# Performance work log

Measured on AMD Instinct MI355X. Metric: run time of the kernel, lower is better.

The kernel has to match this reference:

```python
import jax, jax.numpy as jnp
import numpy as np

C = 256
CI = C // 2  # inter_channels


def conv1x1(x, w, b):
    # x: [B,C,H,W], w: [O,C], b: [O] -> [B,O,H,W]
    return jnp.einsum('bchw,oc->bohw', x, w) + b[None, :, None, None]


def setup_inputs() -> dict:
    key = jax.random.key(0)
    ks = jax.random.split(key, 9)
    B, H, W = 8, 56, 56
    s = 0.02
    return {
        'x': jax.random.normal(ks[0], (B, C, H, W), dtype=jnp.float32),
        'g_w': jax.random.normal(ks[1], (CI, C), dtype=jnp.float32) * s,
        'g_b': jax.random.normal(ks[2], (CI,), dtype=jnp.float32) * s,
        'theta_w': jax.random.normal(ks[3], (CI, C), dtype=jnp.float32) * s,
        'theta_b': jax.random.normal(ks[4], (CI,), dtype=jnp.float32) * s,
        'phi_w': jax.random.normal(ks[5], (CI, C), dtype=jnp.float32) * s,
        'phi_b': jax.random.normal(ks[6], (CI,), dtype=jnp.float32) * s,
        'W_w': jax.random.normal(ks[7], (C, CI), dtype=jnp.float32) * s,
        'W_b': jax.random.normal(ks[8], (C,), dtype=jnp.float32) * s,
    }


def reference(x, g_w, g_b, theta_w, theta_b, phi_w, phi_b, W_w, W_b):
    B, Cc, H, Wd = x.shape
    N = H * Wd
    g_x = conv1x1(x, g_w, g_b).reshape(B, CI, N).transpose(0, 2, 1)        # [B,N,CI]
    theta_x = conv1x1(x, theta_w, theta_b).reshape(B, CI, N).transpose(0, 2, 1)  # [B,N,CI]
    phi_x = conv1x1(x, phi_w, phi_b).reshape(B, CI, N)                     # [B,CI,N]
    f = jnp.einsum('bnc,bcm->bnm', theta_x, phi_x)                         # [B,N,N]
    attn = jax.nn.softmax(f, axis=-1)
    y = jnp.einsum('bnm,bmc->bnc', attn, g_x)                              # [B,N,CI]
    y = y.transpose(0, 2, 1).reshape(B, CI, H, Wd)                         # [B,CI,H,W]
    z = conv1x1(y, W_w, W_b) + x
    return z
```

## Files before the change

kernel.cpp:

```cpp
#include <hip/hip_runtime.h>

#define NB 8
#define C 256
#define CI 128
#define NPIX 3136
#define NT 64
#define NTILES 49
#define NGQ 13
#define NROWT 98
#define NSPLIT 4
#define LOG2E 1.44269504f

typedef unsigned short u16;
typedef unsigned int u32;
typedef __bf16 bf16x8 __attribute__((ext_vector_type(8)));
typedef float f32x4 __attribute__((ext_vector_type(4)));
typedef float f32x16 __attribute__((ext_vector_type(16)));

static __device__ __forceinline__ u16 f2b(float f) {
  union { float f; u32 u; } v; v.f = f;
  u32 r = v.u + 0x7FFFu + ((v.u >> 16) & 1u);
  return (u16)(r >> 16);
}
static __device__ __forceinline__ float b2f(u16 v) {
  union { u32 u; float f; } x; x.u = ((u32)v) << 16; return x.f;
}
static __device__ __forceinline__ u32 cvtpk(float lo, float hi) {
  u32 r;
  asm("v_cvt_pk_bf16_f32 %0, %1, %2" : "=v"(r) : "v"(lo), "v"(hi));
  return r;
}
static __device__ __forceinline__ void swap32(u32& x, u32& y) {
  asm("v_permlane32_swap_b32 %0, %1" : "+v"(x), "+v"(y));
}
static __device__ __forceinline__ void gl16(const void* g, void* l) {
  __builtin_amdgcn_global_load_lds(
      (const __attribute__((address_space(1))) u32*)g,
      (__attribute__((address_space(3))) u32*)l, 16, 0, 0);
}

__global__ __launch_bounds__(256) void k0_convert(
    const float* __restrict__ g_w, const float* __restrict__ th_w,
    const float* __restrict__ ph_w, const float* __restrict__ W_w,
    u16* __restrict__ wcat, u16* __restrict__ Wbf) {
  int i = blockIdx.x * 256 + threadIdx.x;
  if (i < 98304) {
    int o = i >> 8, c = i & 255;
    float v = (o < 128) ? g_w[o * 256 + c]
            : (o < 256) ? th_w[(o - 128) * 256 + c] * LOG2E
                        : ph_w[(o - 256) * 256 + c];
    wcat[i] = f2b(v);
  } else {
    int j = i - 98304;
    Wbf[j] = f2b(W_w[j]);
  }
}

__global__ __launch_bounds__(256) void k1_proj(
    const float* __restrict__ x, const float* __restrict__ g_b,
    const float* __restrict__ th_b, const float* __restrict__ ph_b,
    const u16* __restrict__ wcat, u16* __restrict__ thO,
    u16* __restrict__ phO, u16* __restrict__ gO) {
  __shared__ __align__(16) u16 xT[32 * 264];
  char* xTb = reinterpret_cast<char*>(xT);
  int tid = threadIdx.x;
  int b = blockIdx.x / NROWT, nt = blockIdx.x % NROWT;
  int n0 = nt * 32;
  const float* xb = x + (size_t)b * C * NPIX;
  {
    int c0 = tid >> 3, nq = tid & 7;
    for (int k = 0; k < 8; ++k) {
      int c = c0 + 32 * k;
      float4 xv = *reinterpret_cast<const float4*>(xb + (size_t)c * NPIX + n0 + 4 * nq);
      float vals[4] = {xv.x, xv.y, xv.z, xv.w};
#pragma unroll
      for (int j = 0; j < 4; ++j) {
        int row = 4 * nq + j;
        xT[row * 264 + c] = f2b(vals[j]);
      }
    }
  }
  __syncthreads();
  int wave = tid >> 6, lane = tid & 63;
  int wq = wave & 1, wo = wave >> 1;
  int r = 16 * wq + (lane & 15);
  bf16x8 a[8];
#pragma unroll
  for (int kk = 0; kk < 8; ++kk) {
    int ch = 4 * kk + (lane >> 4);
    a[kk] = *reinterpret_cast<const bf16x8*>(xTb + r * 528 + ch * 16);
  }
  for (int os = 12 * wo; os < 12 * wo + 12; ++os) {
    int o = 16 * os + (lane & 15);
    f32x4 acc = {0.f, 0.f, 0.f, 0.f};
    const u16* wrow = wcat + (size_t)o * 256 + 8 * (lane >> 4);
#pragma unroll
    for (int kk = 0; kk < 8; ++kk) {
      bf16x8 bb = *reinterpret_cast<const bf16x8*>(wrow + 32 * kk);
      acc = __builtin_amdgcn_mfma_f32_16x16x32_bf16(a[kk], bb, acc, 0, 0, 0);
    }
    int p = os >> 3;
    int ol = (os & 7) * 16 + (lane & 15);
    const float* bias = (p == 0) ? g_b : (p == 1) ? th_b : ph_b;
    float bv = bias[ol];
    if (p == 1) bv *= LOG2E;
    int nbase = n0 + 16 * wq + 4 * (lane >> 4);
    if (p == 0) {
      ushort4 pk;
      pk.x = f2b(acc[0] + bv); pk.y = f2b(acc[1] + bv);
      pk.z = f2b(acc[2] + bv); pk.w = f2b(acc[3] + bv);
      *reinterpret_cast<ushort4*>(gO + ((size_t)b * CI + ol) * NPIX + nbase) = pk;
    } else {
      u16* dst = (p == 1) ? thO : phO;
#pragma unroll
      for (int j = 0; j < 4; ++j)
        dst[((size_t)b * NPIX + nbase + j) * CI + ol] = f2b(acc[j] + bv);
    }
  }
}

__global__ __launch_bounds__(512, 2) void k2_attn(
    const u16* __restrict__ th, const u16* __restrict__ ph,
    const u16* __restrict__ gbuf, u16* __restrict__ yp,
    float* __restrict__ lm) {
  __shared__ __align__(16) char lds[65536];
  int tid = threadIdx.x, wave = tid >> 6, lane = tid & 63;
  int h5 = lane >> 5, l31 = lane & 31;
  int bid = blockIdx.x;
  int s = bid & 3, rest = bid >> 2;
  int b = rest / NGQ, ng = rest % NGQ;
  int qbase = ng * 256 + wave * 32;
  if (qbase + 32 > NPIX) qbase = NPIX - 32;
  int ts = (NTILES * s) >> 2, te = (NTILES * (s + 1)) >> 2;

  bf16x8 bth[8];
  {
    const u16* trow = th + ((size_t)b * NPIX + qbase + l31) * CI;
#pragma unroll
    for (int ks = 0; ks < 8; ++ks)
      bth[ks] = *reinterpret_cast<const bf16x8*>(trow + 16 * ks + 8 * h5);
  }
  float lrun = 0.f;
  f32x16 zv;
#pragma unroll
  for (int j = 0; j < 16; ++j) zv[j] = 0.f;
  f32x16 yacc[4];
#pragma unroll
  for (int cb = 0; cb < 4; ++cb)
#pragma unroll
    for (int j = 0; j < 16; ++j) yacc[cb][j] = 0.f;

  auto stage = [&](int buf, int mt) {
    int m0 = mt * NT;
    char* phB = lds + buf * 16384;
    char* gB = lds + 32768 + buf * 16384;
#pragma unroll
    for (int c = 0; c < 2; ++c) {
      int call = wave * 2 + c;
      int o = call * 1024 + lane * 16;
      int row = o >> 8, chl = (o >> 4) & 15;
      int chg = chl ^ (row & 15);
      gl16(ph + ((size_t)(b * NPIX + m0 + row)) * CI + chg * 8, phB + call * 1024);
    }
#pragma unroll
    for (int c = 0; c < 2; ++c) {
      int call = wave * 2 + c;
      int o = call * 1024 + lane * 16;
      int ci = o >> 7, chl = (o >> 4) & 7;
      int chg = chl ^ (ci & 7);
      gl16(gbuf + ((size_t)b * CI + ci) * NPIX + m0 + chg * 8, gB + call * 1024);
    }
  };

  stage(0, ts);
  int cur = 0;
  for (int mt = ts; mt < te; ++mt) {
    bool pre = (mt + 1 < te);
    if (pre) stage(cur ^ 1, mt + 1);
    if (pre) {
      asm volatile("s_waitcnt vmcnt(4)" ::: "memory");
    } else {
      asm volatile("s_waitcnt vmcnt(0)" ::: "memory");
    }
    __builtin_amdgcn_s_barrier();
    __builtin_amdgcn_sched_barrier(0);
    char* phB = lds + cur * 16384;
    char* gB = lds + 32768 + cur * 16384;
    f32x16 sv0, sv1;
    __builtin_amdgcn_s_setprio(1);
    {
      int off = l31 * 256 + ((h5 ^ (l31 & 15)) << 4);
      bf16x8 a0 = *reinterpret_cast<const bf16x8*>(phB + off);
      bf16x8 a1 = *reinterpret_cast<const bf16x8*>(phB + off + 8192);
      sv0 = __builtin_amdgcn_mfma_f32_32x32x16_bf16(a0, bth[0], zv, 0, 0, 0);
      sv1 = __builtin_amdgcn_mfma_f32_32x32x16_bf16(a1, bth[0], zv, 0, 0, 0);
    }
#pragma unroll
    for (int ks = 1; ks < 8; ++ks) {
      int chk = 2 * ks + h5;
      int off = l31 * 256 + ((chk ^ (l31 & 15)) << 4);
      bf16x8 a0 = *reinterpret_cast<const bf16x8*>(phB + off);
      bf16x8 a1 = *reinterpret_cast<const bf16x8*>(phB + off + 8192);
      sv0 = __builtin_amdgcn_mfma_f32_32x32x16_bf16(a0, bth[ks], sv0, 0, 0, 0);
      sv1 = __builtin_amdgcn_mfma_f32_32x32x16_bf16(a1, bth[ks], sv1, 0, 0, 0);
    }
    __builtin_amdgcn_s_setprio(0);
#pragma unroll
    for (int j = 0; j < 16; ++j) {
      sv0[j] = exp2f(sv0[j]);
      sv1[j] = exp2f(sv1[j]);
    }
    float a0 = 0.f, a1 = 0.f, a2 = 0.f, a3 = 0.f;
#pragma unroll
    for (int i = 0; i < 16; i += 4) {
      a0 += sv0[i] + sv1[i];
      a1 += sv0[i + 1] + sv1[i + 1];
      a2 += sv0[i + 2] + sv1[i + 2];
      a3 += sv0[i + 3] + sv1[i + 3];
    }
    lrun += (a0 + a1) + (a2 + a3);
    u32 pk[2][4][2];
#pragma unroll
    for (int t = 0; t < 4; ++t) {
      pk[0][t][0] = cvtpk(sv0[4 * t], sv0[4 * t + 1]);
      pk[0][t][1] = cvtpk(sv0[4 * t + 2], sv0[4 * t + 3]);
      pk[1][t][0] = cvtpk(sv1[4 * t], sv1[4 * t + 1]);
      pk[1][t][1] = cvtpk(sv1[4 * t + 2], sv1[4 * t + 3]);
    }
    __builtin_amdgcn_s_setprio(1);
#pragma unroll
    for (int ks = 0; ks < 4; ++ks) {
      int m2 = ks >> 1, t0 = 2 * (ks & 1);
      swap32(pk[m2][t0][0], pk[m2][t0 + 1][0]);
      swap32(pk[m2][t0][1], pk[m2][t0 + 1][1]);
      union { u32 u[4]; bf16x8 v; } f;
      f.u[0] = pk[m2][t0][0]; f.u[1] = pk[m2][t0][1];
      f.u[2] = pk[m2][t0 + 1][0]; f.u[3] = pk[m2][t0 + 1][1];
      int chk = 2 * ks + h5;
#pragma unroll
      for (int cb = 0; cb < 4; ++cb) {
        int ci = 32 * cb + l31;
        bf16x8 gv = *reinterpret_cast<const bf16x8*>(
            gB + ci * 128 + ((chk ^ (ci & 7)) << 4));
        yacc[cb] = __builtin_amdgcn_mfma_f32_32x32x16_bf16(f.v, gv, yacc[cb], 0, 0, 0);
      }
    }
    __builtin_amdgcn_s_setprio(0);
    __builtin_amdgcn_sched_barrier(0);
    asm volatile("s_waitcnt lgkmcnt(0)" ::: "memory");
    __builtin_amdgcn_s_barrier();
    cur ^= 1;
  }
  lrun += __shfl_xor(lrun, 32);
  u16* ypb = yp + (size_t)(s * NB + b) * NPIX * CI;
#pragma unroll
  for (int cb = 0; cb < 4; ++cb)
#pragma unroll
    for (int j = 0; j < 16; ++j) {
      int n = qbase + (j & 3) + 8 * (j >> 2) + 4 * h5;
      ypb[(size_t)n * CI + 32 * cb + l31] = f2b(yacc[cb][j]);
    }
  if (lane < 32) {
    int n = qbase + l31;
    lm[(size_t)(s * NB + b) * NPIX + n] = lrun;
  }
}

__global__ __launch_bounds__(256) void k3_out(
    const u16* __restrict__ yp, const float* __restrict__ lm,
    const u16* __restrict__ Wbf, const float* __restrict__ W_b,
    const float* __restrict__ x, float* __restrict__ z) {
  int tid = threadIdx.x, wave = tid >> 6, lane = tid & 63;
  int b = blockIdx.x / NROWT, nt = blockIdx.x % NROWT;
  int n0 = nt * 32;
  int q = lane >> 4, l15 = lane & 15;
  int wq = wave & 1, wo = wave >> 1;
  int nfr = n0 + 16 * wq + l15;
  float den = 0.f;
#pragma unroll
  for (int s = 0; s < NSPLIT; ++s)
    den += lm[(size_t)(s * NB + b) * NPIX + nfr];
  float inv = 1.f / den;
  bf16x8 a[4];
#pragma unroll
  for (int kk = 0; kk < 4; ++kk) {
    float ac[8];
#pragma unroll
    for (int e = 0; e < 8; ++e) ac[e] = 0.f;
#pragma unroll
    for (int s = 0; s < NSPLIT; ++s) {
      union { uint4 u4; u16 us[8]; } yv;
      yv.u4 = *reinterpret_cast<const uint4*>(
          yp + (size_t)(s * NB + b) * NPIX * CI + (size_t)nfr * CI + 32 * kk + 8 * q);
#pragma unroll
      for (int e = 0; e < 8; ++e) ac[e] += b2f(yv.us[e]);
    }
    union { u32 u[4]; bf16x8 v; } fa;
    fa.u[0] = cvtpk(ac[0] * inv, ac[1] * inv);
    fa.u[1] = cvtpk(ac[2] * inv, ac[3] * inv);
    fa.u[2] = cvtpk(ac[4] * inv, ac[5] * inv);
    fa.u[3] = cvtpk(ac[6] * inv, ac[7] * inv);
    a[kk] = fa.v;
  }
  for (int os = 8 * wo; os < 8 * wo + 8; ++os) {
    int co = 16 * os + l15;
    f32x4 acc = {0.f, 0.f, 0.f, 0.f};
    const u16* wrow = Wbf + (size_t)co * 128 + 8 * q;
#pragma unroll
    for (int kk = 0; kk < 4; ++kk) {
      bf16x8 bb = *reinterpret_cast<const bf16x8*>(wrow + 32 * kk);
      acc = __builtin_amdgcn_mfma_f32_16x16x32_bf16(a[kk], bb, acc, 0, 0, 0);
    }
    float bw = W_b[co];
    int nb = n0 + 16 * wq + 4 * q;
    size_t off = ((size_t)b * C + co) * NPIX + nb;
    float4 xv = *reinterpret_cast<const float4*>(x + off);
    float4 o;
    o.x = acc[0] + bw + xv.x; o.y = acc[1] + bw + xv.y;
    o.z = acc[2] + bw + xv.z; o.w = acc[3] + bw + xv.w;
    *reinterpret_cast<float4*>(z + off) = o;
  }
}

extern "C" void kernel_launch(void* const* d_in, const int* in_sizes, int n_in,
                              void* d_out, int out_size, void* d_ws, size_t ws_size,
                              hipStream_t stream) {
  const float* x    = (const float*)d_in[0];
  const float* g_w  = (const float*)d_in[1];
  const float* g_b  = (const float*)d_in[2];
  const float* th_w = (const float*)d_in[3];
  const float* th_b = (const float*)d_in[4];
  const float* ph_w = (const float*)d_in[5];
  const float* ph_b = (const float*)d_in[6];
  const float* W_w  = (const float*)d_in[7];
  const float* W_b  = (const float*)d_in[8];
  float* z = (float*)d_out;
  u16* ws = (u16*)d_ws;
  u16* wcat = ws;
  u16* Wbf  = ws + 98304;
  u16* th   = ws + 131072;
  u16* phb  = th + 3211264;
  u16* gbb  = phb + 3211264;
  u16* yp   = gbb + 3211264;
  float* lm = (float*)(ws + 131072 + (size_t)3211264 * 7);
  hipLaunchKernelGGL(k0_convert, dim3(512), dim3(256), 0, stream,
                     g_w, th_w, ph_w, W_w, wcat, Wbf);
  hipLaunchKernelGGL(k1_proj, dim3(NB * NROWT), dim3(256), 0, stream,
                     x, g_b, th_b, ph_b, wcat, th, phb, gbb);
  hipLaunchKernelGGL(k2_attn, dim3(NB * NGQ * NSPLIT), dim3(512), 0, stream,
                     th, phb, gbb, yp, lm);
  hipLaunchKernelGGL(k3_out, dim3(NB * NROWT), dim3(256), 0, stream,
                     yp, lm, Wbf, W_b, x, z);
}
```

Before: 150.8 us.

## Software-pipeline QK^T of next tile with softmax/PV of current tile in attention

The attention kernel now computes the QK^T scores for tile t+1 while doing exp, packing and the PV MFMAs for tile t. It stages phi two tiles ahead and g one tile ahead, using separate staging lambdas. Blocks shrink from 512 to 256 threads (128 queries per block, 25 groups per batch) and the two-blocks-per-CU launch bound is dropped. The aim is to hide MFMA and global-load latency behind the exp work, at the cost of more registers for the second score buffer and more blocks each loading the same K/V tiles.

```diff
diff --git a/kernel.cpp b/kernel.cpp
--- a/kernel.cpp
+++ b/kernel.cpp
@@ -6,7 +6,7 @@
 #define NPIX 3136
 #define NT 64
 #define NTILES 49
-#define NGQ 13
+#define NG 25
 #define NROWT 98
 #define NSPLIT 4
 #define LOG2E 1.44269504f
@@ -119,7 +119,7 @@
   }
 }
 
-__global__ __launch_bounds__(512, 2) void k2_attn(
+__global__ __launch_bounds__(256) void k2_attn(
     const u16* __restrict__ th, const u16* __restrict__ ph,
     const u16* __restrict__ gbuf, u16* __restrict__ yp,
     float* __restrict__ lm) {
@@ -128,8 +128,8 @@
   int h5 = lane >> 5, l31 = lane & 31;
   int bid = blockIdx.x;
   int s = bid & 3, rest = bid >> 2;
-  int b = rest / NGQ, ng = rest % NGQ;
-  int qbase = ng * 256 + wave * 32;
+  int b = rest / NG, ng = rest % NG;
+  int qbase = ng * 128 + wave * 32;
   if (qbase + 32 > NPIX) qbase = NPIX - 32;
   int ts = (NTILES * s) >> 2, te = (NTILES * (s + 1)) >> 2;
 
@@ -150,50 +150,39 @@
 #pragma unroll
     for (int j = 0; j < 16; ++j) yacc[cb][j] = 0.f;
 
-  auto stage = [&](int buf, int mt) {
+  auto stage_phi = [&](int buf, int mt) {
     int m0 = mt * NT;
     char* phB = lds + buf * 16384;
-    char* gB = lds + 32768 + buf * 16384;
-#pragma unroll
-    for (int c = 0; c < 2; ++c) {
-      int call = wave * 2 + c;
+#pragma unroll
+    for (int c = 0; c < 4; ++c) {
+      int call = wave * 4 + c;
       int o = call * 1024 + lane * 16;
       int row = o >> 8, chl = (o >> 4) & 15;
       int chg = chl ^ (row & 15);
       gl16(ph + ((size_t)(b * NPIX + m0 + row)) * CI + chg * 8, phB + call * 1024);
     }
-#pragma unroll
-    for (int c = 0; c < 2; ++c) {
-      int call = wave * 2 + c;
+  };
+  auto stage_g = [&](int buf, int mt) {
+    int m0 = mt * NT;
+    char* gB = lds + 32768 + buf * 16384;
+#pragma unroll
+    for (int c = 0; c < 4; ++c) {
+      int call = wave * 4 + c;
       int o = call * 1024 + lane * 16;
       int ci = o >> 7, chl = (o >> 4) & 7;
       int chg = chl ^ (ci & 7);
       gl16(gbuf + ((size_t)b * CI + ci) * NPIX + m0 + chg * 8, gB + call * 1024);
     }
   };
-
-  stage(0, ts);
-  int cur = 0;
-  for (int mt = ts; mt < te; ++mt) {
-    bool pre = (mt + 1 < te);
-    if (pre) stage(cur ^ 1, mt + 1);
-    if (pre) {
-      asm volatile("s_waitcnt vmcnt(4)" ::: "memory");
-    } else {
-      asm volatile("s_waitcnt vmcnt(0)" ::: "memory");
-    }
-    __builtin_amdgcn_s_barrier();
-    __builtin_amdgcn_sched_barrier(0);
-    char* phB = lds + cur * 16384;
-    char* gB = lds + 32768 + cur * 16384;
-    f32x16 sv0, sv1;
+  auto qk = [&](int buf, f32x16& s0, f32x16& s1) {
+    char* phB = lds + buf * 16384;
     __builtin_amdgcn_s_setprio(1);
     {
       int off = l31 * 256 + ((h5 ^ (l31 & 15)) << 4);
       bf16x8 a0 = *reinterpret_cast<const bf16x8*>(phB + off);
       bf16x8 a1 = *reinterpret_cast<const bf16x8*>(phB + off + 8192);
-      sv0 = __builtin_amdgcn_mfma_f32_32x32x16_bf16(a0, bth[0], zv, 0, 0, 0);
-      sv1 = __builtin_amdgcn_mfma_f32_32x32x16_bf16(a1, bth[0], zv, 0, 0, 0);
+      s0 = __builtin_amdgcn_mfma_f32_32x32x16_bf16(a0, bth[0], zv, 0, 0, 0);
+      s1 = __builtin_amdgcn_mfma_f32_32x32x16_bf16(a1, bth[0], zv, 0, 0, 0);
     }
 #pragma unroll
     for (int ks = 1; ks < 8; ++ks) {
@@ -201,32 +190,42 @@
       int off = l31 * 256 + ((chk ^ (l31 & 15)) << 4);
       bf16x8 a0 = *reinterpret_cast<const bf16x8*>(phB + off);
       bf16x8 a1 = *reinterpret_cast<const bf16x8*>(phB + off + 8192);
-      sv0 = __builtin_amdgcn_mfma_f32_32x32x16_bf16(a0, bth[ks], sv0, 0, 0, 0);
-      sv1 = __builtin_amdgcn_mfma_f32_32x32x16_bf16(a1, bth[ks], sv1, 0, 0, 0);
+      s0 = __builtin_amdgcn_mfma_f32_32x32x16_bf16(a0, bth[ks], s0, 0, 0, 0);
+      s1 = __builtin_amdgcn_mfma_f32_32x32x16_bf16(a1, bth[ks], s1, 0, 0, 0);
     }
     __builtin_amdgcn_s_setprio(0);
+  };
+  auto body = [&](int t, f32x16& c0, f32x16& c1, f32x16& n0v, f32x16& n1v) {
+    asm volatile("s_waitcnt vmcnt(0)" ::: "memory");
+    __builtin_amdgcn_s_barrier();
+    __builtin_amdgcn_sched_barrier(0);
+    int p = (t - ts) & 1;
+    if (t + 1 < te) stage_g(p ^ 1, t + 1);
+    if (t + 2 < te) stage_phi(p, t + 2);
+    if (t + 1 < te) qk(p ^ 1, n0v, n1v);
 #pragma unroll
     for (int j = 0; j < 16; ++j) {
-      sv0[j] = exp2f(sv0[j]);
-      sv1[j] = exp2f(sv1[j]);
+      c0[j] = exp2f(c0[j]);
+      c1[j] = exp2f(c1[j]);
     }
     float a0 = 0.f, a1 = 0.f, a2 = 0.f, a3 = 0.f;
 #pragma unroll
     for (int i = 0; i < 16; i += 4) {
-      a0 += sv0[i] + sv1[i];
-      a1 += sv0[i + 1] + sv1[i + 1];
-      a2 += sv0[i + 2] + sv1[i + 2];
-      a3 += sv0[i + 3] + sv1[i + 3];
+      a0 += c0[i] + c1[i];
+      a1 += c0[i + 1] + c1[i + 1];
+      a2 += c0[i + 2] + c1[i + 2];
+      a3 += c0[i + 3] + c1[i + 3];
     }
     lrun += (a0 + a1) + (a2 + a3);
     u32 pk[2][4][2];
 #pragma unroll
-    for (int t = 0; t < 4; ++t) {
-      pk[0][t][0] = cvtpk(sv0[4 * t], sv0[4 * t + 1]);
-      pk[0][t][1] = cvtpk(sv0[4 * t + 2], sv0[4 * t + 3]);
-      pk[1][t][0] = cvtpk(sv1[4 * t], sv1[4 * t + 1]);
-      pk[1][t][1] = cvtpk(sv1[4 * t + 2], sv1[4 * t + 3]);
-    }
+    for (int tt = 0; tt < 4; ++tt) {
+      pk[0][tt][0] = cvtpk(c0[4 * tt], c0[4 * tt + 1]);
+      pk[0][tt][1] = cvtpk(c0[4 * tt + 2], c0[4 * tt + 3]);
+      pk[1][tt][0] = cvtpk(c1[4 * tt], c1[4 * tt + 1]);
+      pk[1][tt][1] = cvtpk(c1[4 * tt + 2], c1[4 * tt + 3]);
+    }
+    char* gB = lds + 32768 + p * 16384;
     __builtin_amdgcn_s_setprio(1);
 #pragma unroll
     for (int ks = 0; ks < 4; ++ks) {
@@ -246,11 +245,26 @@
       }
     }
     __builtin_amdgcn_s_setprio(0);
-    __builtin_amdgcn_sched_barrier(0);
-    asm volatile("s_waitcnt lgkmcnt(0)" ::: "memory");
-    __builtin_amdgcn_s_barrier();
-    cur ^= 1;
-  }
+  };
+
+  f32x16 sA0, sA1, sB0, sB1;
+  stage_phi(0, ts);
+  stage_g(0, ts);
+  if (ts + 1 < te) {
+    stage_phi(1, ts + 1);
+    asm volatile("s_waitcnt vmcnt(8)" ::: "memory");
+  } else {
+    asm volatile("s_waitcnt vmcnt(4)" ::: "memory");
+  }
+  __builtin_amdgcn_s_barrier();
+  __builtin_amdgcn_sched_barrier(0);
+  qk(0, sA0, sA1);
+
+  for (int t = ts; t < te; t += 2) {
+    body(t, sA0, sA1, sB0, sB1);
+    if (t + 1 < te) body(t + 1, sB0, sB1, sA0, sA1);
+  }
+
   lrun += __shfl_xor(lrun, 32);
   u16* ypb = yp + (size_t)(s * NB + b) * NPIX * CI;
 #pragma unroll
@@ -347,7 +361,7 @@
                      g_w, th_w, ph_w, W_w, wcat, Wbf);
   hipLaunchKernelGGL(k1_proj, dim3(NB * NROWT), dim3(256), 0, stream,
                      x, g_b, th_b, ph_b, wcat, th, phb, gbb);
-  hipLaunchKernelGGL(k2_attn, dim3(NB * NGQ * NSPLIT), dim3(512), 0, stream,
+  hipLaunchKernelGGL(k2_attn, dim3(NB * NG * NSPLIT), dim3(256), 0, stream,
                      th, phb, gbb, yp, lm);
   hipLaunchKernelGGL(k3_out, dim3(NB * NROWT), dim3(256), 0, stream,
                      yp, lm, Wbf, W_b, x, z);
```

Measured after the change: 180.9 us. 20.0% more time.

## Read phi directly from global and shrink attention blocks to four waves

Applied to the files above, without the earlier changes.

The attention kernel no longer stages phi tiles in LDS. Each wave loads its phi fragments straight from global memory, and only the g tile is double-buffered in LDS. The block is halved to 256 threads covering 128 queries with a 32KB LDS footprint, which doubles the grid. The g prefetch is moved after the QK^T MFMAs and the trailing per-iteration barrier is dropped, cutting LDS traffic and synchronisation. In exchange, phi is now read redundantly by every wave through L1/L2 with uncoalesced row-strided loads, and the last query group overlaps with its neighbour and recomputes some rows.

```diff
diff --git a/kernel.cpp b/kernel.cpp
--- a/kernel.cpp
+++ b/kernel.cpp
@@ -6,7 +6,7 @@
 #define NPIX 3136
 #define NT 64
 #define NTILES 49
-#define NGQ 13
+#define NG 25
 #define NROWT 98
 #define NSPLIT 4
 #define LOG2E 1.44269504f
@@ -119,17 +119,17 @@
   }
 }
 
-__global__ __launch_bounds__(512, 2) void k2_attn(
+__global__ __launch_bounds__(256) void k2_attn(
     const u16* __restrict__ th, const u16* __restrict__ ph,
     const u16* __restrict__ gbuf, u16* __restrict__ yp,
     float* __restrict__ lm) {
-  __shared__ __align__(16) char lds[65536];
+  __shared__ __align__(16) char lds[32768];
   int tid = threadIdx.x, wave = tid >> 6, lane = tid & 63;
   int h5 = lane >> 5, l31 = lane & 31;
   int bid = blockIdx.x;
   int s = bid & 3, rest = bid >> 2;
-  int b = rest / NGQ, ng = rest % NGQ;
-  int qbase = ng * 256 + wave * 32;
+  int b = rest / NG, ng = rest % NG;
+  int qbase = ng * 128 + wave * 32;
   if (qbase + 32 > NPIX) qbase = NPIX - 32;
   int ts = (NTILES * s) >> 2, te = (NTILES * (s + 1)) >> 2;
 
@@ -150,21 +150,12 @@
 #pragma unroll
     for (int j = 0; j < 16; ++j) yacc[cb][j] = 0.f;
 
-  auto stage = [&](int buf, int mt) {
+  auto stage_g = [&](int buf, int mt) {
     int m0 = mt * NT;
-    char* phB = lds + buf * 16384;
-    char* gB = lds + 32768 + buf * 16384;
-#pragma unroll
-    for (int c = 0; c < 2; ++c) {
-      int call = wave * 2 + c;
-      int o = call * 1024 + lane * 16;
-      int row = o >> 8, chl = (o >> 4) & 15;
-      int chg = chl ^ (row & 15);
-      gl16(ph + ((size_t)(b * NPIX + m0 + row)) * CI + chg * 8, phB + call * 1024);
-    }
-#pragma unroll
-    for (int c = 0; c < 2; ++c) {
-      int call = wave * 2 + c;
+    char* gB = lds + buf * 16384;
+#pragma unroll
+    for (int c = 0; c < 4; ++c) {
+      int call = wave * 4 + c;
       int o = call * 1024 + lane * 16;
       int ci = o >> 7, chl = (o >> 4) & 7;
       int chg = chl ^ (ci & 7);
@@ -172,39 +163,35 @@
     }
   };
 
-  stage(0, ts);
+  stage_g(0, ts);
   int cur = 0;
   for (int mt = ts; mt < te; ++mt) {
-    bool pre = (mt + 1 < te);
-    if (pre) stage(cur ^ 1, mt + 1);
-    if (pre) {
-      asm volatile("s_waitcnt vmcnt(4)" ::: "memory");
-    } else {
-      asm volatile("s_waitcnt vmcnt(0)" ::: "memory");
-    }
+    asm volatile("s_waitcnt vmcnt(0)" ::: "memory");
     __builtin_amdgcn_s_barrier();
     __builtin_amdgcn_sched_barrier(0);
-    char* phB = lds + cur * 16384;
-    char* gB = lds + 32768 + cur * 16384;
+    const u16* phbase = ph + ((size_t)b * NPIX + mt * NT) * CI;
     f32x16 sv0, sv1;
     __builtin_amdgcn_s_setprio(1);
     {
-      int off = l31 * 256 + ((h5 ^ (l31 & 15)) << 4);
-      bf16x8 a0 = *reinterpret_cast<const bf16x8*>(phB + off);
-      bf16x8 a1 = *reinterpret_cast<const bf16x8*>(phB + off + 8192);
+      int chk = h5;
+      const u16* pr = phbase + l31 * CI + chk * 8;
+      bf16x8 a0 = *reinterpret_cast<const bf16x8*>(pr);
+      bf16x8 a1 = *reinterpret_cast<const bf16x8*>(pr + 32 * CI);
       sv0 = __builtin_amdgcn_mfma_f32_32x32x16_bf16(a0, bth[0], zv, 0, 0, 0);
       sv1 = __builtin_amdgcn_mfma_f32_32x32x16_bf16(a1, bth[0], zv, 0, 0, 0);
     }
 #pragma unroll
     for (int ks = 1; ks < 8; ++ks) {
       int chk = 2 * ks + h5;
-      int off = l31 * 256 + ((chk ^ (l31 & 15)) << 4);
-      bf16x8 a0 = *reinterpret_cast<const bf16x8*>(phB + off);
-      bf16x8 a1 = *reinterpret_cast<const bf16x8*>(phB + off + 8192);
+      const u16* pr = phbase + l31 * CI + chk * 8;
+      bf16x8 a0 = *reinterpret_cast<const bf16x8*>(pr);
+      bf16x8 a1 = *reinterpret_cast<const bf16x8*>(pr + 32 * CI);
       sv0 = __builtin_amdgcn_mfma_f32_32x32x16_bf16(a0, bth[ks], sv0, 0, 0, 0);
       sv1 = __builtin_amdgcn_mfma_f32_32x32x16_bf16(a1, bth[ks], sv1, 0, 0, 0);
     }
     __builtin_amdgcn_s_setprio(0);
+    __builtin_amdgcn_sched_barrier(0);
+    if (mt + 1 < te) stage_g(cur ^ 1, mt + 1);
 #pragma unroll
     for (int j = 0; j < 16; ++j) {
       sv0[j] = exp2f(sv0[j]);
@@ -227,6 +214,7 @@
       pk[1][t][0] = cvtpk(sv1[4 * t], sv1[4 * t + 1]);
       pk[1][t][1] = cvtpk(sv1[4 * t + 2], sv1[4 * t + 3]);
     }
+    char* gB = lds + cur * 16384;
     __builtin_amdgcn_s_setprio(1);
 #pragma unroll
     for (int ks = 0; ks < 4; ++ks) {
@@ -246,9 +234,6 @@
       }
     }
     __builtin_amdgcn_s_setprio(0);
-    __builtin_amdgcn_sched_barrier(0);
-    asm volatile("s_waitcnt lgkmcnt(0)" ::: "memory");
-    __builtin_amdgcn_s_barrier();
     cur ^= 1;
   }
   lrun += __shfl_xor(lrun, 32);
@@ -347,7 +332,7 @@
                      g_w, th_w, ph_w, W_w, wcat, Wbf);
   hipLaunchKernelGGL(k1_proj, dim3(NB * NROWT), dim3(256), 0, stream,
                      x, g_b, th_b, ph_b, wcat, th, phb, gbb);
-  hipLaunchKernelGGL(k2_attn, dim3(NB * NGQ * NSPLIT), dim3(512), 0, stream,
+  hipLaunchKernelGGL(k2_attn, dim3(NB * NG * NSPLIT), dim3(256), 0, stream,
                      th, phb, gbb, yp, lm);
   hipLaunchKernelGGL(k3_out, dim3(NB * NROWT), dim3(256), 0, stream,
                      yp, lm, Wbf, W_b, x, z);
```

After: 194.3 us. 28.9% more time.

## Shrink attention blocks, single-buffer g tile, and rewrite projection as per-wave kernel

Applied to the files above, without the earlier changes.

The projection kernel becomes one wave per 16-pixel column tile. It loads x directly into registers with strided scalar loads, drops the LDS transpose and swaps MFMA operand roles so output writes change layout. The attention kernel goes from 512 to 256 threads with 128 queries per block, so there are more blocks. Its g tile is now single-buffered and staged after the loop-top barrier, with split waitcnts so the phi GEMM overlaps the g load and the end-of-iteration barrier is removed. This reduces LDS use and aims for better occupancy and overlap, but it risks uncoalesced x loads, and the single-buffered g tile may be overwritten while slower waves are still reading the previous one.

```diff
diff --git a/kernel.cpp b/kernel.cpp
--- a/kernel.cpp
+++ b/kernel.cpp
@@ -6,7 +6,8 @@
 #define NPIX 3136
 #define NT 64
 #define NTILES 49
-#define NGQ 13
+#define NG 25
+#define NCOLT 196
 #define NROWT 98
 #define NSPLIT 4
 #define LOG2E 1.44269504f
@@ -56,80 +57,72 @@
   }
 }
 
-__global__ __launch_bounds__(256) void k1_proj(
+__global__ __launch_bounds__(64) void k1_proj(
     const float* __restrict__ x, const float* __restrict__ g_b,
     const float* __restrict__ th_b, const float* __restrict__ ph_b,
     const u16* __restrict__ wcat, u16* __restrict__ thO,
     u16* __restrict__ phO, u16* __restrict__ gO) {
-  __shared__ __align__(16) u16 xT[32 * 264];
-  char* xTb = reinterpret_cast<char*>(xT);
-  int tid = threadIdx.x;
-  int b = blockIdx.x / NROWT, nt = blockIdx.x % NROWT;
-  int n0 = nt * 32;
+  int lane = threadIdx.x;
+  int bid = blockIdx.x;
+  int b = bid / NCOLT, ct = bid % NCOLT;
+  int n0 = ct * 16;
+  int q = lane >> 4, l15 = lane & 15;
+  int n = n0 + l15;
   const float* xb = x + (size_t)b * C * NPIX;
-  {
-    int c0 = tid >> 3, nq = tid & 7;
-    for (int k = 0; k < 8; ++k) {
-      int c = c0 + 32 * k;
-      float4 xv = *reinterpret_cast<const float4*>(xb + (size_t)c * NPIX + n0 + 4 * nq);
-      float vals[4] = {xv.x, xv.y, xv.z, xv.w};
-#pragma unroll
-      for (int j = 0; j < 4; ++j) {
-        int row = 4 * nq + j;
-        xT[row * 264 + c] = f2b(vals[j]);
-      }
-    }
-  }
-  __syncthreads();
-  int wave = tid >> 6, lane = tid & 63;
-  int wq = wave & 1, wo = wave >> 1;
-  int r = 16 * wq + (lane & 15);
-  bf16x8 a[8];
+  bf16x8 xf[8];
 #pragma unroll
   for (int kk = 0; kk < 8; ++kk) {
-    int ch = 4 * kk + (lane >> 4);
-    a[kk] = *reinterpret_cast<const bf16x8*>(xTb + r * 528 + ch * 16);
-  }
-  for (int os = 12 * wo; os < 12 * wo + 12; ++os) {
-    int o = 16 * os + (lane & 15);
+    const float* xc = xb + (size_t)(32 * kk + 8 * q) * NPIX + n;
+    float v[8];
+#pragma unroll
+    for (int e = 0; e < 8; ++e) v[e] = xc[(size_t)e * NPIX];
+    union { u32 u[4]; bf16x8 v8; } p;
+    p.u[0] = cvtpk(v[0], v[1]); p.u[1] = cvtpk(v[2], v[3]);
+    p.u[2] = cvtpk(v[4], v[5]); p.u[3] = cvtpk(v[6], v[7]);
+    xf[kk] = p.v8;
+  }
+  for (int os = 0; os < 24; ++os) {
+    int p_ = os >> 3;
+    int olb = (os & 7) * 16;
     f32x4 acc = {0.f, 0.f, 0.f, 0.f};
-    const u16* wrow = wcat + (size_t)o * 256 + 8 * (lane >> 4);
+    const u16* wrow = wcat + (size_t)(16 * os + l15) * 256 + 8 * q;
 #pragma unroll
     for (int kk = 0; kk < 8; ++kk) {
-      bf16x8 bb = *reinterpret_cast<const bf16x8*>(wrow + 32 * kk);
-      acc = __builtin_amdgcn_mfma_f32_16x16x32_bf16(a[kk], bb, acc, 0, 0, 0);
-    }
-    int p = os >> 3;
-    int ol = (os & 7) * 16 + (lane & 15);
-    const float* bias = (p == 0) ? g_b : (p == 1) ? th_b : ph_b;
-    float bv = bias[ol];
-    if (p == 1) bv *= LOG2E;
-    int nbase = n0 + 16 * wq + 4 * (lane >> 4);
-    if (p == 0) {
+      bf16x8 aw = *reinterpret_cast<const bf16x8*>(wrow + 32 * kk);
+      acc = __builtin_amdgcn_mfma_f32_16x16x32_bf16(aw, xf[kk], acc, 0, 0, 0);
+    }
+    const float* bias = (p_ == 0) ? g_b : (p_ == 1) ? th_b : ph_b;
+    float4 bv = *reinterpret_cast<const float4*>(bias + olb + 4 * q);
+    if (p_ == 1) { bv.x *= LOG2E; bv.y *= LOG2E; bv.z *= LOG2E; bv.w *= LOG2E; }
+    if (p_ == 0) {
+      int o = olb + 4 * q;
+      u16* gb = gO + ((size_t)b * CI + o) * NPIX + n;
+      gb[0] = f2b(acc[0] + bv.x);
+      gb[NPIX] = f2b(acc[1] + bv.y);
+      gb[2 * NPIX] = f2b(acc[2] + bv.z);
+      gb[3 * NPIX] = f2b(acc[3] + bv.w);
+    } else {
+      u16* dst = (p_ == 1) ? thO : phO;
       ushort4 pk;
-      pk.x = f2b(acc[0] + bv); pk.y = f2b(acc[1] + bv);
-      pk.z = f2b(acc[2] + bv); pk.w = f2b(acc[3] + bv);
-      *reinterpret_cast<ushort4*>(gO + ((size_t)b * CI + ol) * NPIX + nbase) = pk;
-    } else {
-      u16* dst = (p == 1) ? thO : phO;
-#pragma unroll
-      for (int j = 0; j < 4; ++j)
-        dst[((size_t)b * NPIX + nbase + j) * CI + ol] = f2b(acc[j] + bv);
-    }
-  }
-}
-
-__global__ __launch_bounds__(512, 2) void k2_attn(
+      pk.x = f2b(acc[0] + bv.x); pk.y = f2b(acc[1] + bv.y);
+      pk.z = f2b(acc[2] + bv.z); pk.w = f2b(acc[3] + bv.w);
+      *reinterpret_cast<ushort4*>(dst + ((size_t)b * NPIX + n) * CI + olb + 4 * q) = pk;
+    }
+  }
+}
+
+__global__ __launch_bounds__(256) void k2_attn(
     const u16* __restrict__ th, const u16* __restrict__ ph,
     const u16* __restrict__ gbuf, u16* __restrict__ yp,
     float* __restrict__ lm) {
-  __shared__ __align__(16) char lds[65536];
+  __shared__ __align__(16) char lds[49152];
+  char* gB = lds + 32768;
   int tid = threadIdx.x, wave = tid >> 6, lane = tid & 63;
   int h5 = lane >> 5, l31 = lane & 31;
   int bid = blockIdx.x;
   int s = bid & 3, rest = bid >> 2;
-  int b = rest / NGQ, ng = rest % NGQ;
-  int qbase = ng * 256 + wave * 32;
+  int b = rest / NG, ng = rest % NG;
+  int qbase = ng * 128 + wave * 32;
   if (qbase + 32 > NPIX) qbase = NPIX - 32;
   int ts = (NTILES * s) >> 2, te = (NTILES * (s + 1)) >> 2;
 
@@ -150,21 +143,23 @@
 #pragma unroll
     for (int j = 0; j < 16; ++j) yacc[cb][j] = 0.f;
 
-  auto stage = [&](int buf, int mt) {
+  auto stage_phi = [&](int buf, int mt) {
     int m0 = mt * NT;
     char* phB = lds + buf * 16384;
-    char* gB = lds + 32768 + buf * 16384;
-#pragma unroll
-    for (int c = 0; c < 2; ++c) {
-      int call = wave * 2 + c;
+#pragma unroll
+    for (int c = 0; c < 4; ++c) {
+      int call = wave * 4 + c;
       int o = call * 1024 + lane * 16;
       int row = o >> 8, chl = (o >> 4) & 15;
       int chg = chl ^ (row & 15);
       gl16(ph + ((size_t)(b * NPIX + m0 + row)) * CI + chg * 8, phB + call * 1024);
     }
-#pragma unroll
-    for (int c = 0; c < 2; ++c) {
-      int call = wave * 2 + c;
+  };
+  auto stage_g = [&](int mt) {
+    int m0 = mt * NT;
+#pragma unroll
+    for (int c = 0; c < 4; ++c) {
+      int call = wave * 4 + c;
       int o = call * 1024 + lane * 16;
       int ci = o >> 7, chl = (o >> 4) & 7;
       int chg = chl ^ (ci & 7);
@@ -172,20 +167,21 @@
     }
   };
 
-  stage(0, ts);
+  stage_phi(0, ts);
   int cur = 0;
   for (int mt = ts; mt < te; ++mt) {
-    bool pre = (mt + 1 < te);
-    if (pre) stage(cur ^ 1, mt + 1);
-    if (pre) {
-      asm volatile("s_waitcnt vmcnt(4)" ::: "memory");
-    } else {
-      asm volatile("s_waitcnt vmcnt(0)" ::: "memory");
-    }
     __builtin_amdgcn_s_barrier();
     __builtin_amdgcn_sched_barrier(0);
+    stage_g(mt);
+    bool pre = (mt + 1 < te);
+    if (pre) stage_phi(cur ^ 1, mt + 1);
+    if (pre) {
+      asm volatile("s_waitcnt vmcnt(8)" ::: "memory");
+    } else {
+      asm volatile("s_waitcnt vmcnt(4)" ::: "memory");
+    }
+    __builtin_amdgcn_sched_barrier(0);
     char* phB = lds + cur * 16384;
-    char* gB = lds + 32768 + cur * 16384;
     f32x16 sv0, sv1;
     __builtin_amdgcn_s_setprio(1);
     {
@@ -227,6 +223,12 @@
       pk[1][t][0] = cvtpk(sv1[4 * t], sv1[4 * t + 1]);
       pk[1][t][1] = cvtpk(sv1[4 * t + 2], sv1[4 * t + 3]);
     }
+    if (pre) {
+      asm volatile("s_waitcnt vmcnt(4)" ::: "memory");
+    } else {
+      asm volatile("s_waitcnt vmcnt(0)" ::: "memory");
+    }
+    __builtin_amdgcn_sched_barrier(0);
     __builtin_amdgcn_s_setprio(1);
 #pragma unroll
     for (int ks = 0; ks < 4; ++ks) {
@@ -246,9 +248,6 @@
       }
     }
     __builtin_amdgcn_s_setprio(0);
-    __builtin_amdgcn_sched_barrier(0);
-    asm volatile("s_waitcnt lgkmcnt(0)" ::: "memory");
-    __builtin_amdgcn_s_barrier();
     cur ^= 1;
   }
   lrun += __shfl_xor(lrun, 32);
@@ -345,9 +344,9 @@
   float* lm = (float*)(ws + 131072 + (size_t)3211264 * 7);
   hipLaunchKernelGGL(k0_convert, dim3(512), dim3(256), 0, stream,
                      g_w, th_w, ph_w, W_w, wcat, Wbf);
-  hipLaunchKernelGGL(k1_proj, dim3(NB * NROWT), dim3(256), 0, stream,
+  hipLaunchKernelGGL(k1_proj, dim3(NB * NCOLT), dim3(64), 0, stream,
                      x, g_b, th_b, ph_b, wcat, th, phb, gbb);
-  hipLaunchKernelGGL(k2_attn, dim3(NB * NGQ * NSPLIT), dim3(512), 0, stream,
+  hipLaunchKernelGGL(k2_attn, dim3(NB * NG * NSPLIT), dim3(256), 0, stream,
                      th, phb, gbb, yp, lm);
   hipLaunchKernelGGL(k3_out, dim3(NB * NROWT), dim3(256), 0, stream,
                      yp, lm, Wbf, W_b, x, z);
```

Measured after the change: 153.9 us. +2.1%, slower.
